# Performance work log

Hardware: AMD Instinct MI355X
Metric: run time of the kernel (lower is better)

## Reference

```python
import jax, jax.numpy as jnp
import numpy as np

EPS = 0.05
THRESH = 1e-6
MAX_ITER = 100


def _l2norm(x):
    # matches torch F.normalize(dim=-1): x / max(||x||, 1e-12)
    n = jnp.sqrt(jnp.sum(x * x, axis=-1, keepdims=True))
    return x / jnp.maximum(n, 1e-12)


def setup_inputs() -> dict:
    key = jax.random.key(0)
    kq, kk, kv = jax.random.split(key, 3)
    B, N, D = 8, 1024, 64
    return {
        "q": jax.random.normal(kq, (B, N, D), dtype=jnp.float32),
        "k": jax.random.normal(kk, (B, N, D), dtype=jnp.float32),
        "V": jax.random.normal(kv, (B, N, D), dtype=jnp.float32),
    }


def reference(q, k, V):
    B, N, D = q.shape
    Q = _l2norm(q)
    Kn = _l2norm(k)
    # cost matrix: 1 - cosine similarity, shape (B, N, N)
    C = 1.0 - jnp.einsum("bnd,bmd->bnm", Q, Kn)

    log_mu = jnp.full((B, N), jnp.log(1.0 / N + 1e-8), dtype=C.dtype)
    log_nu = log_mu

    def kernel(u, v):
        # (-C + u_i + v_j) / eps, shape (B, N, N)
        return (-C + u[:, :, None] + v[:, None, :]) / EPS

    def step(carry, _):
        u, v, done = carry
        u0 = u
        u_new = EPS * (log_mu - jax.scipy.special.logsumexp(kernel(u, v), axis=2)) + u
        v_new = EPS * (log_nu - jax.scipy.special.logsumexp(kernel(u_new, v), axis=1)) + v
        err = jnp.mean(jnp.abs(u_new - u0))
        # replicate torch early-break: once converged, freeze u, v
        u = jnp.where(done, u, u_new)
        v = jnp.where(done, v, v_new)
        done = jnp.logical_or(done, err < THRESH)
        return (u, v, done), None

    u0 = jnp.zeros((B, N), dtype=C.dtype)
    v0 = jnp.zeros((B, N), dtype=C.dtype)
    (u, v, _), _ = jax.lax.scan(
        jax.checkpoint(step), (u0, v0, jnp.array(False)), None, length=MAX_ITER
    )

    T = jnp.exp(kernel(u, v))  # transport plan (B, N, N)
    out = jnp.einsum("bnm,bmd->bnd", T, V) + V
    return out
```

## Files before the change

kernel.cpp:

```cpp
#include <hip/hip_runtime.h>
#include <math.h>

#define BB 8
#define NN 1024
#define DD 64
#define EPSF 0.05f
#define MAX_ITER 100
#define ERR_FX_THRESH 8590u
#define SCALE_ 28.853900817779268f
#define EPSLN2_ 0.034657359027997264f
#define NBLK 256
#define NPER 32

typedef __attribute__((ext_vector_type(8))) short short8;
typedef __attribute__((ext_vector_type(4))) float f32x4;

static __device__ __forceinline__ float fexp2(float x) { return __builtin_amdgcn_exp2f(x); }
static __device__ __forceinline__ float flog2(float x) { return __builtin_amdgcn_logf(x); }
static __device__ __forceinline__ float bflo(unsigned u) { return __uint_as_float(u << 16); }
static __device__ __forceinline__ unsigned short bf16rne(float x) {
    unsigned u = __float_as_uint(x);
    u += 0x7fffu + ((u >> 16) & 1u);
    return (unsigned short)(u >> 16);
}
__device__ __forceinline__ float wave_sum64(float x) {
#pragma unroll
    for (int off = 1; off < 64; off <<= 1) x += __shfl_xor(x, off);
    return x;
}

#define CNT64IDX(p, b) ((b) * 200 + (p))

__global__ __launch_bounds__(256) void cost_kernel(const float* __restrict__ q,
                                                   const float* __restrict__ k,
                                                   unsigned short* __restrict__ M,
                                                   unsigned short* __restrict__ MT) {
    __shared__ __align__(16) float Qs[64][65];
    __shared__ __align__(16) float Ks[64][65];
    __shared__ float qin[64];
    __shared__ float kin[64];
    __shared__ __align__(16) unsigned short Qb[64][72];
    __shared__ __align__(16) unsigned short Kb[64][72];
    int b = blockIdx.z;
    int i0 = blockIdx.y * 64, j0 = blockIdx.x * 64;
    const float* Qp = q + ((size_t)b * NN + i0) * DD;
    const float* Kp = k + ((size_t)b * NN + j0) * DD;
    int tid = threadIdx.x;
#pragma unroll
    for (int kk = 0; kk < 4; ++kk) {
        int c = tid + 256 * kk;
        int row = c >> 4;
        int c4 = c & 15;
        float4 qv = ((const float4*)(Qp + row * DD))[c4];
        Qs[row][c4 * 4 + 0] = qv.x; Qs[row][c4 * 4 + 1] = qv.y;
        Qs[row][c4 * 4 + 2] = qv.z; Qs[row][c4 * 4 + 3] = qv.w;
        float4 kv = ((const float4*)(Kp + row * DD))[c4];
        Ks[row][c4 * 4 + 0] = kv.x; Ks[row][c4 * 4 + 1] = kv.y;
        Ks[row][c4 * 4 + 2] = kv.z; Ks[row][c4 * 4 + 3] = kv.w;
    }
    __syncthreads();
    if (tid < 64) {
        float ss = 0.f;
#pragma unroll 16
        for (int d = 0; d < 64; ++d) ss += Qs[tid][d] * Qs[tid][d];
        qin[tid] = 1.0f / fmaxf(sqrtf(ss), 1e-12f);
    } else if (tid < 128) {
        int r = tid - 64;
        float ss = 0.f;
#pragma unroll 16
        for (int d = 0; d < 64; ++d) ss += Ks[r][d] * Ks[r][d];
        kin[r] = 1.0f / fmaxf(sqrtf(ss), 1e-12f);
    }
    __syncthreads();
    {
        int row = tid >> 2, d0 = (tid & 3) * 16;
        float qs = qin[row], ks = kin[row];
#pragma unroll
        for (int p = 0; p < 4; ++p) {
            int d = d0 + p * 4;
            uint2 t;
            t.x = (unsigned)bf16rne(Qs[row][d + 0] * qs) | ((unsigned)bf16rne(Qs[row][d + 1] * qs) << 16);
            t.y = (unsigned)bf16rne(Qs[row][d + 2] * qs) | ((unsigned)bf16rne(Qs[row][d + 3] * qs) << 16);
            *(uint2*)&Qb[row][d] = t;
            t.x = (unsigned)bf16rne(Ks[row][d + 0] * ks) | ((unsigned)bf16rne(Ks[row][d + 1] * ks) << 16);
            t.y = (unsigned)bf16rne(Ks[row][d + 2] * ks) | ((unsigned)bf16rne(Ks[row][d + 3] * ks) << 16);
            *(uint2*)&Kb[row][d] = t;
        }
    }
    __syncthreads();
    unsigned short* Ms = (unsigned short*)&Qs[0][0];
    int w = tid >> 6, lane = tid & 63;
    int m = lane & 15, qq = lane >> 4;
    int rloc = w * 16;
    short8 a0 = *(const short8*)&Qb[rloc + m][qq * 8];
    short8 a1 = *(const short8*)&Qb[rloc + m][qq * 8 + 32];
    f32x4 acc[4];
#pragma unroll
    for (int nt = 0; nt < 4; ++nt) {
        short8 b0 = *(const short8*)&Kb[nt * 16 + m][qq * 8];
        short8 b1 = *(const short8*)&Kb[nt * 16 + m][qq * 8 + 32];
        f32x4 z = {0.f, 0.f, 0.f, 0.f};
        z = __builtin_amdgcn_mfma_f32_16x16x32_bf16(a0, b0, z, 0, 0, 0);
        acc[nt] = __builtin_amdgcn_mfma_f32_16x16x32_bf16(a1, b1, z, 0, 0, 0);
    }
#pragma unroll
    for (int nt = 0; nt < 4; ++nt) {
        int gj = j0 + nt * 16 + m;
        unsigned short us[4];
#pragma unroll
        for (int r = 0; r < 4; ++r)
            us[r] = bf16rne(fexp2((acc[nt][r] - 1.0f) * SCALE_));
#pragma unroll
        for (int r = 0; r < 4; ++r)
            Ms[(rloc + qq * 4 + r) * 72 + nt * 16 + m] = us[r];
        uint2 t;
        t.x = (unsigned)us[0] | ((unsigned)us[1] << 16);
        t.y = (unsigned)us[2] | ((unsigned)us[3] << 16);
        *(uint2*)(MT + ((size_t)b << 20) + ((size_t)gj << 10) + i0 + rloc + qq * 4) = t;
    }
    __syncthreads();
#pragma unroll
    for (int s = 0; s < 2; ++s) {
        int idx = tid + 256 * s;
        int row = idx >> 3, seg = idx & 7;
        *(uint4*)(M + ((size_t)b << 20) + ((size_t)(i0 + row) << 10) + j0 + seg * 8) =
            *(const uint4*)&Ms[row * 72 + seg * 8];
    }
}

#define ACC8(U4, base)                                              \
    s0 = fmaf(bflo(U4.x), wrg[base + 0], s0);                       \
    s1 = fmaf(__uint_as_float(U4.x), wrg[base + 1], s1);            \
    s0 = fmaf(bflo(U4.y), wrg[base + 2], s0);                       \
    s1 = fmaf(__uint_as_float(U4.y), wrg[base + 3], s1);            \
    s0 = fmaf(bflo(U4.z), wrg[base + 4], s0);                       \
    s1 = fmaf(__uint_as_float(U4.z), wrg[base + 5], s1);            \
    s0 = fmaf(bflo(U4.w), wrg[base + 6], s0);                       \
    s1 = fmaf(__uint_as_float(U4.w), wrg[base + 7], s1);

__global__ __launch_bounds__(256, 1) void sink_coop(const unsigned short* __restrict__ M,
                                                    const unsigned short* __restrict__ MT,
                                                    float* __restrict__ u,
                                                    float* __restrict__ v,
                                                    unsigned long long* __restrict__ cnt64,
                                                    float eln) {
    __shared__ __align__(16) float sw[1280];
    __shared__ float sdel[4];
    __shared__ int sflag;
    int tid = threadIdx.x;
    int w = tid >> 6, lane = tid & 63;
    int b = blockIdx.x & 7;
    int slice = blockIdx.x >> 3;
    int rbase = slice * 32 + w * 8;
    const unsigned short* Mb  = M  + ((size_t)b << 20);
    const unsigned short* MTb = MT + ((size_t)b << 20);
    float* ub = u + (b << 10);
    float* vb = v + (b << 10);

    uint4 mA[8], mB[8], nA[8], nB[8];
#pragma unroll
    for (int r = 0; r < 8; ++r) {
        const uint4* rp = (const uint4*)(Mb + ((size_t)(rbase + r) << 10));
        mA[r] = rp[lane * 2];
        mB[r] = rp[lane * 2 + 1];
        const uint4* tp = (const uint4*)(MTb + ((size_t)(rbase + r) << 10));
        nA[r] = tp[lane * 2];
        nB[r] = tp[lane * 2 + 1];
    }

    float uprev[8];
#pragma unroll
    for (int r = 0; r < 8; ++r) uprev[r] = 0.f;

    unsigned myerr = 0xffffffffu;

    for (int t = 0; t < MAX_ITER; ++t) {
        {
            float4 ex;
            ex.x = fexp2(__hip_atomic_load(vb + tid * 4 + 0, __ATOMIC_RELAXED, __HIP_MEMORY_SCOPE_AGENT) * SCALE_);
            ex.y = fexp2(__hip_atomic_load(vb + tid * 4 + 1, __ATOMIC_RELAXED, __HIP_MEMORY_SCOPE_AGENT) * SCALE_);
            ex.z = fexp2(__hip_atomic_load(vb + tid * 4 + 2, __ATOMIC_RELAXED, __HIP_MEMORY_SCOPE_AGENT) * SCALE_);
            ex.w = fexp2(__hip_atomic_load(vb + tid * 4 + 3, __ATOMIC_RELAXED, __HIP_MEMORY_SCOPE_AGENT) * SCALE_);
            *(float4*)&sw[tid * 4 + 4 * (tid >> 2)] = ex;
            __syncthreads();
            float wrg[16];
            *(float4*)&wrg[0]  = *(const float4*)&sw[lane * 20 + 0];
            *(float4*)&wrg[4]  = *(const float4*)&sw[lane * 20 + 4];
            *(float4*)&wrg[8]  = *(const float4*)&sw[lane * 20 + 8];
            *(float4*)&wrg[12] = *(const float4*)&sw[lane * 20 + 12];
            float del = 0.f;
#pragma unroll
            for (int rr = 0; rr < 8; ++rr) {
                float s0 = 0.f, s1 = 0.f;
                ACC8(mA[rr], 0)
                ACC8(mB[rr], 8)
                float s = wave_sum64(s0 + s1);
                float un = eln - EPSLN2_ * flog2(s);
                del += fabsf(un - uprev[rr]);
                uprev[rr] = un;
                if (lane == 0)
                    __hip_atomic_store(ub + rbase + rr, un, __ATOMIC_RELAXED, __HIP_MEMORY_SCOPE_AGENT);
            }
            if (lane == 0) sdel[w] = del;
            asm volatile("s_waitcnt vmcnt(0)" ::: "memory");
            __syncthreads();
            if (tid == 0) {
                float dsum = sdel[0] + sdel[1] + sdel[2] + sdel[3];
                unsigned dfx = (unsigned)fminf(dsum * 1048576.0f, 6.0e7f) + 1u;
                unsigned long long* c = cnt64 + CNT64IDX(2 * t, b);
                unsigned long long tot =
                    __hip_atomic_fetch_add(c, (1ULL << 32) | (unsigned long long)dfx,
                                           __ATOMIC_RELAXED, __HIP_MEMORY_SCOPE_AGENT) +
                    ((1ULL << 32) | (unsigned long long)dfx);
                while ((unsigned)(tot >> 32) < NPER) {
                    __builtin_amdgcn_s_sleep(1);
                    tot = __hip_atomic_load(c, __ATOMIC_RELAXED, __HIP_MEMORY_SCOPE_AGENT);
                }
                myerr = (unsigned)tot;
            }
            __syncthreads();
        }
        {
            float4 ex;
            ex.x = fexp2(__hip_atomic_load(ub + tid * 4 + 0, __ATOMIC_RELAXED, __HIP_MEMORY_SCOPE_AGENT) * SCALE_);
            ex.y = fexp2(__hip_atomic_load(ub + tid * 4 + 1, __ATOMIC_RELAXED, __HIP_MEMORY_SCOPE_AGENT) * SCALE_);
            ex.z = fexp2(__hip_atomic_load(ub + tid * 4 + 2, __ATOMIC_RELAXED, __HIP_MEMORY_SCOPE_AGENT) * SCALE_);
            ex.w = fexp2(__hip_atomic_load(ub + tid * 4 + 3, __ATOMIC_RELAXED, __HIP_MEMORY_SCOPE_AGENT) * SCALE_);
            *(float4*)&sw[tid * 4 + 4 * (tid >> 2)] = ex;
            __syncthreads();
            float wrg[16];
            *(float4*)&wrg[0]  = *(const float4*)&sw[lane * 20 + 0];
            *(float4*)&wrg[4]  = *(const float4*)&sw[lane * 20 + 4];
            *(float4*)&wrg[8]  = *(const float4*)&sw[lane * 20 + 8];
            *(float4*)&wrg[12] = *(const float4*)&sw[lane * 20 + 12];
#pragma unroll
            for (int rr = 0; rr < 8; ++rr) {
                float s0 = 0.f, s1 = 0.f;
                ACC8(nA[rr], 0)
                ACC8(nB[rr], 8)
                float s = wave_sum64(s0 + s1);
                float vn = eln - EPSLN2_ * flog2(s);
                if (lane == 0)
                    __hip_atomic_store(vb + rbase + rr, vn, __ATOMIC_RELAXED, __HIP_MEMORY_SCOPE_AGENT);
            }
            asm volatile("s_waitcnt vmcnt(0)" ::: "memory");
            __syncthreads();
            if (tid == 0) {
                unsigned long long* c = cnt64 + CNT64IDX(2 * t + 1, b);
                unsigned long long tot =
                    __hip_atomic_fetch_add(c, 1ULL << 32, __ATOMIC_RELAXED, __HIP_MEMORY_SCOPE_AGENT) +
                    (1ULL << 32);
                while ((unsigned)(tot >> 32) < NPER) {
                    __builtin_amdgcn_s_sleep(1);
                    tot = __hip_atomic_load(c, __ATOMIC_RELAXED, __HIP_MEMORY_SCOPE_AGENT);
                }
                int brk = 0;
                if (myerr < ERR_FX_THRESH) {
                    unsigned long long s = 0;
                    for (int bb = 0; bb < 8; ++bb) {
                        unsigned long long tv = __hip_atomic_load(cnt64 + CNT64IDX(2 * t, bb),
                                                                  __ATOMIC_RELAXED, __HIP_MEMORY_SCOPE_AGENT);
                        while ((unsigned)(tv >> 32) < NPER) {
                            __builtin_amdgcn_s_sleep(1);
                            tv = __hip_atomic_load(cnt64 + CNT64IDX(2 * t, bb),
                                                   __ATOMIC_RELAXED, __HIP_MEMORY_SCOPE_AGENT);
                        }
                        s += (unsigned long long)(unsigned)tv;
                    }
                    brk = (s < (unsigned long long)ERR_FX_THRESH);
                }
                sflag = brk;
            }
            __syncthreads();
            if (sflag) break;
        }
    }
}

__global__ __launch_bounds__(256) void wt_kernel(const float* __restrict__ V,
                                                 const float* __restrict__ v,
                                                 unsigned short* __restrict__ WT) {
    __shared__ __align__(16) float Vs[64][65];
    __shared__ float wj[64];
    int b = blockIdx.x & 7, jt = blockIdx.x >> 3;
    int j0 = jt * 64;
    int tid = threadIdx.x;
    const float* Vb = V + ((size_t)b << 16) + ((size_t)j0 << 6);
#pragma unroll
    for (int c = 0; c < 4; ++c) {
        int idx = tid + 256 * c;
        int row = idx >> 4, c4 = idx & 15;
        float4 x = ((const float4*)(Vb + row * 64))[c4];
        Vs[row][c4 * 4 + 0] = x.x; Vs[row][c4 * 4 + 1] = x.y;
        Vs[row][c4 * 4 + 2] = x.z; Vs[row][c4 * 4 + 3] = x.w;
    }
    if (tid < 64) wj[tid] = fexp2(v[(b << 10) + j0 + tid] * SCALE_);
    __syncthreads();
    int d = tid >> 2, qd = tid & 3;
    unsigned pk[8];
#pragma unroll
    for (int p = 0; p < 8; ++p) {
        int j = qd * 16 + p * 2;
        unsigned lo = bf16rne(Vs[j][d] * wj[j]);
        unsigned hi = bf16rne(Vs[j + 1][d] * wj[j + 1]);
        pk[p] = lo | (hi << 16);
    }
    unsigned short* dst = WT + ((size_t)b << 16) + ((size_t)d << 10) + j0 + qd * 16;
    ((uint4*)dst)[0] = make_uint4(pk[0], pk[1], pk[2], pk[3]);
    ((uint4*)dst)[1] = make_uint4(pk[4], pk[5], pk[6], pk[7]);
}

__global__ __launch_bounds__(256) void gemm_final(const unsigned short* __restrict__ M,
                                                  const unsigned short* __restrict__ WT,
                                                  const float* __restrict__ u,
                                                  const float* __restrict__ V,
                                                  float* __restrict__ out) {
    __shared__ float sa[32];
    int tid = threadIdx.x;
    int w = tid >> 6, lane = tid & 63;
    int b = blockIdx.x & 7, mt = blockIdx.x >> 3;
    if (tid < 32) sa[tid] = fexp2(u[(b << 10) + mt * 32 + tid] * SCALE_);
    __syncthreads();
    int m = lane & 15, q = lane >> 4;
    int rloc = (w & 1) * 16;
    int nbase = (w >> 1) * 32;
    const unsigned short* Ma = M + ((size_t)b << 20) + ((size_t)(mt * 32 + rloc + m) << 10) + q * 8;
    const unsigned short* W0 = WT + ((size_t)b << 16) + ((size_t)(nbase + m) << 10) + q * 8;
    const unsigned short* W1 = W0 + (16 << 10);
    f32x4 acc0 = {0.f, 0.f, 0.f, 0.f}, acc1 = {0.f, 0.f, 0.f, 0.f};
#pragma unroll 4
    for (int k0 = 0; k0 < NN; k0 += 32) {
        short8 af = *(const short8*)(Ma + k0);
        short8 b0 = *(const short8*)(W0 + k0);
        short8 b1 = *(const short8*)(W1 + k0);
        acc0 = __builtin_amdgcn_mfma_f32_16x16x32_bf16(af, b0, acc0, 0, 0, 0);
        acc1 = __builtin_amdgcn_mfma_f32_16x16x32_bf16(af, b1, acc1, 0, 0, 0);
    }
#pragma unroll
    for (int r = 0; r < 4; ++r) {
        int lrow = rloc + q * 4 + r;
        int gm = mt * 32 + lrow;
        float a = sa[lrow];
        size_t base = (((size_t)b << 10) + gm) * DD;
        int n0 = nbase + m;
        out[base + n0]      = fmaf(a, acc0[r], V[base + n0]);
        out[base + n0 + 16] = fmaf(a, acc1[r], V[base + n0 + 16]);
    }
}

extern "C" void kernel_launch(void* const* d_in, const int* in_sizes, int n_in,
                              void* d_out, int out_size, void* d_ws, size_t ws_size,
                              hipStream_t stream) {
    const float* q = (const float*)d_in[0];
    const float* k = (const float*)d_in[1];
    const float* V = (const float*)d_in[2];
    float* out = (float*)d_out;

    char* ws = (char*)d_ws;
    const size_t MB16 = (size_t)BB * NN * NN * sizeof(unsigned short);
    unsigned short* M  = (unsigned short*)ws;
    unsigned short* MT = (unsigned short*)(ws + MB16);
    unsigned short* WT = MT;
    float* u   = (float*)(ws + 2 * MB16);
    float* v   = u + BB * NN;
    unsigned long long* cnt64 = (unsigned long long*)(v + BB * NN);

    size_t zbytes = (size_t)(2 * BB * NN) * 4 + 1600 * 8;
    hipMemsetAsync(u, 0, zbytes, stream);

    cost_kernel<<<dim3(16, 16, 8), 256, 0, stream>>>(q, k, M, MT);

    float eln = EPSF * logf(1.0f / NN + 1e-8f);
    sink_coop<<<dim3(NBLK), dim3(256), 0, stream>>>(M, MT, u, v, cnt64, eln);

    wt_kernel<<<128, 256, 0, stream>>>(V, v, WT);
    gemm_final<<<256, 256, 0, stream>>>(M, WT, u, V, out);
}
```

Baseline: 183.8 us.

## Replace barrier counters with epoch-tagged fixed-point u/v words for dataflow sync

The Sinkhorn cooperative kernel no longer uses per-half-iteration grid barriers. Each u/v entry is stored as a 32-bit word holding a 7-bit iteration tag and a 25-bit fixed-point value, so consumers spin on the data itself until all tags match. Wave 0 polls and decodes the values and hands them to the other waves through LDS flags. The convergence check is deferred by one iteration and overlapped with the next half-step. Together these remove barrier latency and block-wide syncthreads. The cost is quantized u/v values clamped to ±8, reliance on tag wraparound staying under 128 iterations, and busy-waiting in the LDS spin loops.

```diff
diff --git a/kernel.cpp b/kernel.cpp
--- a/kernel.cpp
+++ b/kernel.cpp
@@ -10,7 +10,9 @@
 #define SCALE_ 28.853900817779268f
 #define EPSLN2_ 0.034657359027997264f
 #define NBLK 256
-#define NPER 32
+#define NPERW 128
+#define QSCALE 2097152.0f
+#define DECE ((float)(28.853900817779268 / 2097152.0))
 
 typedef __attribute__((ext_vector_type(8))) short short8;
 typedef __attribute__((ext_vector_type(4))) float f32x4;
@@ -28,8 +30,11 @@
     for (int off = 1; off < 64; off <<= 1) x += __shfl_xor(x, off);
     return x;
 }
-
-#define CNT64IDX(p, b) ((b) * 200 + (p))
+static __device__ __forceinline__ float dec_exp(unsigned w) {
+    int fx = ((int)(w << 7)) >> 7;
+    return fexp2((float)fx * DECE);
+}
+
 
 __global__ __launch_bounds__(256) void cost_kernel(const float* __restrict__ q,
                                                    const float* __restrict__ k,
@@ -140,13 +145,13 @@
 
 __global__ __launch_bounds__(256, 1) void sink_coop(const unsigned short* __restrict__ M,
                                                     const unsigned short* __restrict__ MT,
-                                                    float* __restrict__ u,
-                                                    float* __restrict__ v,
+                                                    unsigned* __restrict__ ut,
+                                                    unsigned* __restrict__ vt,
                                                     unsigned long long* __restrict__ cnt64,
                                                     float eln) {
-    __shared__ __align__(16) float sw[1280];
-    __shared__ float sdel[4];
-    __shared__ int sflag;
+    __shared__ __align__(16) float bufU[1280];
+    __shared__ __align__(16) float bufV[1280];
+    __shared__ int flagU, flagV;
     int tid = threadIdx.x;
     int w = tid >> 6, lane = tid & 63;
     int b = blockIdx.x & 7;
@@ -154,8 +159,12 @@
     int rbase = slice * 32 + w * 8;
     const unsigned short* Mb  = M  + ((size_t)b << 20);
     const unsigned short* MTb = MT + ((size_t)b << 20);
-    float* ub = u + (b << 10);
-    float* vb = v + (b << 10);
+    unsigned* ub = ut + (b << 10);
+    unsigned* vb = vt + (b << 10);
+    const unsigned* vp = vb + lane * 16;
+    const unsigned* up = ub + lane * 16;
+
+    if (tid == 0) { flagU = 0; flagV = 0; }
 
     uint4 mA[8], mB[8], nA[8], nB[8];
 #pragma unroll
@@ -167,118 +176,149 @@
         nA[r] = tp[lane * 2];
         nB[r] = tp[lane * 2 + 1];
     }
+    __syncthreads();
 
     float uprev[8];
 #pragma unroll
     for (int r = 0; r < 8; ++r) uprev[r] = 0.f;
 
-    unsigned myerr = 0xffffffffu;
-
     for (int t = 0; t < MAX_ITER; ++t) {
-        {
-            float4 ex;
-            ex.x = fexp2(__hip_atomic_load(vb + tid * 4 + 0, __ATOMIC_RELAXED, __HIP_MEMORY_SCOPE_AGENT) * SCALE_);
-            ex.y = fexp2(__hip_atomic_load(vb + tid * 4 + 1, __ATOMIC_RELAXED, __HIP_MEMORY_SCOPE_AGENT) * SCALE_);
-            ex.z = fexp2(__hip_atomic_load(vb + tid * 4 + 2, __ATOMIC_RELAXED, __HIP_MEMORY_SCOPE_AGENT) * SCALE_);
-            ex.w = fexp2(__hip_atomic_load(vb + tid * 4 + 3, __ATOMIC_RELAXED, __HIP_MEMORY_SCOPE_AGENT) * SCALE_);
-            *(float4*)&sw[tid * 4 + 4 * (tid >> 2)] = ex;
-            __syncthreads();
-            float wrg[16];
-            *(float4*)&wrg[0]  = *(const float4*)&sw[lane * 20 + 0];
-            *(float4*)&wrg[4]  = *(const float4*)&sw[lane * 20 + 4];
-            *(float4*)&wrg[8]  = *(const float4*)&sw[lane * 20 + 8];
-            *(float4*)&wrg[12] = *(const float4*)&sw[lane * 20 + 12];
-            float del = 0.f;
-#pragma unroll
-            for (int rr = 0; rr < 8; ++rr) {
-                float s0 = 0.f, s1 = 0.f;
-                ACC8(mA[rr], 0)
-                ACC8(mB[rr], 8)
-                float s = wave_sum64(s0 + s1);
-                float un = eln - EPSLN2_ * flog2(s);
-                del += fabsf(un - uprev[rr]);
-                uprev[rr] = un;
-                if (lane == 0)
-                    __hip_atomic_store(ub + rbase + rr, un, __ATOMIC_RELAXED, __HIP_MEMORY_SCOPE_AGENT);
-            }
-            if (lane == 0) sdel[w] = del;
-            asm volatile("s_waitcnt vmcnt(0)" ::: "memory");
-            __syncthreads();
-            if (tid == 0) {
-                float dsum = sdel[0] + sdel[1] + sdel[2] + sdel[3];
-                unsigned dfx = (unsigned)fminf(dsum * 1048576.0f, 6.0e7f) + 1u;
-                unsigned long long* c = cnt64 + CNT64IDX(2 * t, b);
-                unsigned long long tot =
-                    __hip_atomic_fetch_add(c, (1ULL << 32) | (unsigned long long)dfx,
-                                           __ATOMIC_RELAXED, __HIP_MEMORY_SCOPE_AGENT) +
-                    ((1ULL << 32) | (unsigned long long)dfx);
-                while ((unsigned)(tot >> 32) < NPER) {
-                    __builtin_amdgcn_s_sleep(1);
-                    tot = __hip_atomic_load(c, __ATOMIC_RELAXED, __HIP_MEMORY_SCOPE_AGENT);
+        unsigned tgv = (unsigned)t;
+        unsigned tgu = (unsigned)(t + 1);
+        float wrg[16];
+        if (w == 0) {
+            unsigned wv[16];
+            for (;;) {
+                unsigned bad = 0;
+#pragma unroll
+                for (int i = 0; i < 16; ++i)
+                    wv[i] = __hip_atomic_load(vp + i, __ATOMIC_RELAXED, __HIP_MEMORY_SCOPE_AGENT);
+#pragma unroll
+                for (int i = 0; i < 16; ++i) bad |= (wv[i] >> 25) ^ tgv;
+                if (!bad) break;
+                __builtin_amdgcn_s_sleep(1);
+            }
+#pragma unroll
+            for (int i = 0; i < 4; ++i) {
+                float4 f;
+                f.x = dec_exp(wv[i * 4 + 0]); f.y = dec_exp(wv[i * 4 + 1]);
+                f.z = dec_exp(wv[i * 4 + 2]); f.w = dec_exp(wv[i * 4 + 3]);
+                *(float4*)&bufU[lane * 20 + i * 4] = f;
+                wrg[i * 4 + 0] = f.x; wrg[i * 4 + 1] = f.y;
+                wrg[i * 4 + 2] = f.z; wrg[i * 4 + 3] = f.w;
+            }
+            if (lane == 0)
+                __hip_atomic_store(&flagU, t + 1, __ATOMIC_RELEASE, __HIP_MEMORY_SCOPE_WORKGROUP);
+        } else {
+            while (__hip_atomic_load(&flagU, __ATOMIC_ACQUIRE, __HIP_MEMORY_SCOPE_WORKGROUP) < t + 1) {}
+#pragma unroll
+            for (int i = 0; i < 4; ++i) {
+                float4 f = *(const float4*)&bufU[lane * 20 + i * 4];
+                wrg[i * 4 + 0] = f.x; wrg[i * 4 + 1] = f.y;
+                wrg[i * 4 + 2] = f.z; wrg[i * 4 + 3] = f.w;
+            }
+        }
+        float del = 0.f;
+#pragma unroll
+        for (int rr = 0; rr < 8; ++rr) {
+            float s0 = 0.f, s1 = 0.f;
+            ACC8(mA[rr], 0)
+            ACC8(mB[rr], 8)
+            float s = wave_sum64(s0 + s1);
+            float un = eln - EPSLN2_ * flog2(s);
+            del += fabsf(un - uprev[rr]);
+            uprev[rr] = un;
+            if (lane == 0) {
+                float uq = fminf(fmaxf(un, -7.99f), 7.99f);
+                int fx = (int)rintf(uq * QSCALE);
+                unsigned word = (tgu << 25) | ((unsigned)fx & 0x1FFFFFFu);
+                __hip_atomic_store(ub + rbase + rr, word, __ATOMIC_RELAXED, __HIP_MEMORY_SCOPE_AGENT);
+            }
+        }
+        if (lane == 0) {
+            unsigned dfx = (unsigned)fminf(del * 1048576.0f, 1.5e7f) + 1u;
+            __hip_atomic_fetch_add(cnt64 + (size_t)t * 8 + b,
+                                   (1ULL << 32) | (unsigned long long)dfx,
+                                   __ATOMIC_RELAXED, __HIP_MEMORY_SCOPE_AGENT);
+        }
+        unsigned long long e[8];
+        if (t) {
+#pragma unroll
+            for (int i = 0; i < 8; ++i)
+                e[i] = __hip_atomic_load(cnt64 + (size_t)(t - 1) * 8 + i,
+                                         __ATOMIC_RELAXED, __HIP_MEMORY_SCOPE_AGENT);
+        }
+        if (w == 0) {
+            unsigned wu[16];
+            for (;;) {
+                unsigned bad = 0;
+#pragma unroll
+                for (int i = 0; i < 16; ++i)
+                    wu[i] = __hip_atomic_load(up + i, __ATOMIC_RELAXED, __HIP_MEMORY_SCOPE_AGENT);
+#pragma unroll
+                for (int i = 0; i < 16; ++i) bad |= (wu[i] >> 25) ^ tgu;
+                if (!bad) break;
+                __builtin_amdgcn_s_sleep(1);
+            }
+#pragma unroll
+            for (int i = 0; i < 4; ++i) {
+                float4 f;
+                f.x = dec_exp(wu[i * 4 + 0]); f.y = dec_exp(wu[i * 4 + 1]);
+                f.z = dec_exp(wu[i * 4 + 2]); f.w = dec_exp(wu[i * 4 + 3]);
+                *(float4*)&bufV[lane * 20 + i * 4] = f;
+                wrg[i * 4 + 0] = f.x; wrg[i * 4 + 1] = f.y;
+                wrg[i * 4 + 2] = f.z; wrg[i * 4 + 3] = f.w;
+            }
+            if (lane == 0)
+                __hip_atomic_store(&flagV, t + 1, __ATOMIC_RELEASE, __HIP_MEMORY_SCOPE_WORKGROUP);
+        } else {
+            while (__hip_atomic_load(&flagV, __ATOMIC_ACQUIRE, __HIP_MEMORY_SCOPE_WORKGROUP) < t + 1) {}
+#pragma unroll
+            for (int i = 0; i < 4; ++i) {
+                float4 f = *(const float4*)&bufV[lane * 20 + i * 4];
+                wrg[i * 4 + 0] = f.x; wrg[i * 4 + 1] = f.y;
+                wrg[i * 4 + 2] = f.z; wrg[i * 4 + 3] = f.w;
+            }
+        }
+#pragma unroll
+        for (int rr = 0; rr < 8; ++rr) {
+            float s0 = 0.f, s1 = 0.f;
+            ACC8(nA[rr], 0)
+            ACC8(nB[rr], 8)
+            float s = wave_sum64(s0 + s1);
+            float vn = eln - EPSLN2_ * flog2(s);
+            if (lane == 0) {
+                float vq = fminf(fmaxf(vn, -7.99f), 7.99f);
+                int fx = (int)rintf(vq * QSCALE);
+                unsigned word = (tgu << 25) | ((unsigned)fx & 0x1FFFFFFu);
+                __hip_atomic_store(vb + rbase + rr, word, __ATOMIC_RELAXED, __HIP_MEMORY_SCOPE_AGENT);
+            }
+        }
+        if (t) {
+            unsigned long long s = 0;
+            for (;;) {
+                unsigned mn = 0xffffffffu;
+                s = 0;
+#pragma unroll
+                for (int i = 0; i < 8; ++i) {
+                    unsigned c = (unsigned)(e[i] >> 32);
+                    if (c < mn) mn = c;
+                    s += (unsigned long long)(unsigned)(e[i] & 0xffffffffULL);
                 }
-                myerr = (unsigned)tot;
-            }
-            __syncthreads();
-        }
-        {
-            float4 ex;
-            ex.x = fexp2(__hip_atomic_load(ub + tid * 4 + 0, __ATOMIC_RELAXED, __HIP_MEMORY_SCOPE_AGENT) * SCALE_);
-            ex.y = fexp2(__hip_atomic_load(ub + tid * 4 + 1, __ATOMIC_RELAXED, __HIP_MEMORY_SCOPE_AGENT) * SCALE_);
-            ex.z = fexp2(__hip_atomic_load(ub + tid * 4 + 2, __ATOMIC_RELAXED, __HIP_MEMORY_SCOPE_AGENT) * SCALE_);
-            ex.w = fexp2(__hip_atomic_load(ub + tid * 4 + 3, __ATOMIC_RELAXED, __HIP_MEMORY_SCOPE_AGENT) * SCALE_);
-            *(float4*)&sw[tid * 4 + 4 * (tid >> 2)] = ex;
-            __syncthreads();
-            float wrg[16];
-            *(float4*)&wrg[0]  = *(const float4*)&sw[lane * 20 + 0];
-            *(float4*)&wrg[4]  = *(const float4*)&sw[lane * 20 + 4];
-            *(float4*)&wrg[8]  = *(const float4*)&sw[lane * 20 + 8];
-            *(float4*)&wrg[12] = *(const float4*)&sw[lane * 20 + 12];
-#pragma unroll
-            for (int rr = 0; rr < 8; ++rr) {
-                float s0 = 0.f, s1 = 0.f;
-                ACC8(nA[rr], 0)
-                ACC8(nB[rr], 8)
-                float s = wave_sum64(s0 + s1);
-                float vn = eln - EPSLN2_ * flog2(s);
-                if (lane == 0)
-                    __hip_atomic_store(vb + rbase + rr, vn, __ATOMIC_RELAXED, __HIP_MEMORY_SCOPE_AGENT);
-            }
-            asm volatile("s_waitcnt vmcnt(0)" ::: "memory");
-            __syncthreads();
-            if (tid == 0) {
-                unsigned long long* c = cnt64 + CNT64IDX(2 * t + 1, b);
-                unsigned long long tot =
-                    __hip_atomic_fetch_add(c, 1ULL << 32, __ATOMIC_RELAXED, __HIP_MEMORY_SCOPE_AGENT) +
-                    (1ULL << 32);
-                while ((unsigned)(tot >> 32) < NPER) {
-                    __builtin_amdgcn_s_sleep(1);
-                    tot = __hip_atomic_load(c, __ATOMIC_RELAXED, __HIP_MEMORY_SCOPE_AGENT);
-                }
-                int brk = 0;
-                if (myerr < ERR_FX_THRESH) {
-                    unsigned long long s = 0;
-                    for (int bb = 0; bb < 8; ++bb) {
-                        unsigned long long tv = __hip_atomic_load(cnt64 + CNT64IDX(2 * t, bb),
-                                                                  __ATOMIC_RELAXED, __HIP_MEMORY_SCOPE_AGENT);
-                        while ((unsigned)(tv >> 32) < NPER) {
-                            __builtin_amdgcn_s_sleep(1);
-                            tv = __hip_atomic_load(cnt64 + CNT64IDX(2 * t, bb),
-                                                   __ATOMIC_RELAXED, __HIP_MEMORY_SCOPE_AGENT);
-                        }
-                        s += (unsigned long long)(unsigned)tv;
-                    }
-                    brk = (s < (unsigned long long)ERR_FX_THRESH);
-                }
-                sflag = brk;
-            }
-            __syncthreads();
-            if (sflag) break;
+                if (mn >= NPERW) break;
+                __builtin_amdgcn_s_sleep(1);
+#pragma unroll
+                for (int i = 0; i < 8; ++i)
+                    e[i] = __hip_atomic_load(cnt64 + (size_t)(t - 1) * 8 + i,
+                                             __ATOMIC_RELAXED, __HIP_MEMORY_SCOPE_AGENT);
+            }
+            if (s < (unsigned long long)ERR_FX_THRESH) break;
         }
     }
 }
 
 __global__ __launch_bounds__(256) void wt_kernel(const float* __restrict__ V,
-                                                 const float* __restrict__ v,
+                                                 const unsigned* __restrict__ vt,
                                                  unsigned short* __restrict__ WT) {
     __shared__ __align__(16) float Vs[64][65];
     __shared__ float wj[64];
@@ -294,7 +334,7 @@
         Vs[row][c4 * 4 + 0] = x.x; Vs[row][c4 * 4 + 1] = x.y;
         Vs[row][c4 * 4 + 2] = x.z; Vs[row][c4 * 4 + 3] = x.w;
     }
-    if (tid < 64) wj[tid] = fexp2(v[(b << 10) + j0 + tid] * SCALE_);
+    if (tid < 64) wj[tid] = dec_exp(vt[(b << 10) + j0 + tid]);
     __syncthreads();
     int d = tid >> 2, qd = tid & 3;
     unsigned pk[8];
@@ -312,14 +352,14 @@
 
 __global__ __launch_bounds__(256) void gemm_final(const unsigned short* __restrict__ M,
                                                   const unsigned short* __restrict__ WT,
-                                                  const float* __restrict__ u,
+                                                  const unsigned* __restrict__ ut,
                                                   const float* __restrict__ V,
                                                   float* __restrict__ out) {
     __shared__ float sa[32];
     int tid = threadIdx.x;
     int w = tid >> 6, lane = tid & 63;
     int b = blockIdx.x & 7, mt = blockIdx.x >> 3;
-    if (tid < 32) sa[tid] = fexp2(u[(b << 10) + mt * 32 + tid] * SCALE_);
+    if (tid < 32) sa[tid] = dec_exp(ut[(b << 10) + mt * 32 + tid]);
     __syncthreads();
     int m = lane & 15, q = lane >> 4;
     int rloc = (w & 1) * 16;
@@ -361,18 +401,18 @@
     unsigned short* M  = (unsigned short*)ws;
     unsigned short* MT = (unsigned short*)(ws + MB16);
     unsigned short* WT = MT;
-    float* u   = (float*)(ws + 2 * MB16);
-    float* v   = u + BB * NN;
-    unsigned long long* cnt64 = (unsigned long long*)(v + BB * NN);
-
-    size_t zbytes = (size_t)(2 * BB * NN) * 4 + 1600 * 8;
-    hipMemsetAsync(u, 0, zbytes, stream);
+    unsigned* ut = (unsigned*)(ws + 2 * MB16);
+    unsigned* vt = ut + BB * NN;
+    unsigned long long* cnt64 = (unsigned long long*)(vt + BB * NN);
+
+    size_t zbytes = (size_t)(2 * BB * NN) * 4 + 800 * 8;
+    hipMemsetAsync(ut, 0, zbytes, stream);
 
     cost_kernel<<<dim3(16, 16, 8), 256, 0, stream>>>(q, k, M, MT);
 
     float eln = EPSF * logf(1.0f / NN + 1e-8f);
-    sink_coop<<<dim3(NBLK), dim3(256), 0, stream>>>(M, MT, u, v, cnt64, eln);
-
-    wt_kernel<<<128, 256, 0, stream>>>(V, v, WT);
-    gemm_final<<<256, 256, 0, stream>>>(M, WT, u, V, out);
-}
+    sink_coop<<<dim3(NBLK), dim3(256), 0, stream>>>(M, MT, ut, vt, cnt64, eln);
+
+    wt_kernel<<<128, 256, 0, stream>>>(V, vt, WT);
+    gemm_final<<<256, 256, 0, stream>>>(M, WT, ut, V, out);
+}
```

Measured after the change: 448.4 us. 144% more time.

## Replace per-block syncthreads barriers with LDS arrival counters and per-wave spinning

Applied to the files above, without the earlier changes.

Each wave now posts its error contribution and arrival into shared-memory atomic counters. The last-arriving wave issues the global grid-barrier atomic, and every wave spins on the global counter itself, so the two __syncthreads around the thread-0 barrier are gone. The exp-weight staging buffer is split into separate U and V buffers so consecutive phases do not overwrite each other without a block barrier. This is meant to cut intra-block barrier latency in the 200-phase cooperative loop, at the cost of four times as many waves polling global memory. The lack of acquire ordering between waves and the lower per-wave clamp on the error value may raise correctness or memory-ordering risks.

```diff
diff --git a/kernel.cpp b/kernel.cpp
--- a/kernel.cpp
+++ b/kernel.cpp
@@ -144,9 +144,10 @@
                                                     float* __restrict__ v,
                                                     unsigned long long* __restrict__ cnt64,
                                                     float eln) {
-    __shared__ __align__(16) float sw[1280];
-    __shared__ float sdel[4];
-    __shared__ int sflag;
+    __shared__ __align__(16) float bufU[1280];
+    __shared__ __align__(16) float bufV[1280];
+    __shared__ unsigned arr[2];
+    __shared__ unsigned ldsdel;
     int tid = threadIdx.x;
     int w = tid >> 6, lane = tid & 63;
     int b = blockIdx.x & 7;
@@ -157,6 +158,8 @@
     float* ub = u + (b << 10);
     float* vb = v + (b << 10);
 
+    if (tid == 0) { arr[0] = 0u; arr[1] = 0u; ldsdel = 0u; }
+
     uint4 mA[8], mB[8], nA[8], nB[8];
 #pragma unroll
     for (int r = 0; r < 8; ++r) {
@@ -167,6 +170,7 @@
         nA[r] = tp[lane * 2];
         nB[r] = tp[lane * 2 + 1];
     }
+    __syncthreads();
 
     float uprev[8];
 #pragma unroll
@@ -181,13 +185,13 @@
             ex.y = fexp2(__hip_atomic_load(vb + tid * 4 + 1, __ATOMIC_RELAXED, __HIP_MEMORY_SCOPE_AGENT) * SCALE_);
             ex.z = fexp2(__hip_atomic_load(vb + tid * 4 + 2, __ATOMIC_RELAXED, __HIP_MEMORY_SCOPE_AGENT) * SCALE_);
             ex.w = fexp2(__hip_atomic_load(vb + tid * 4 + 3, __ATOMIC_RELAXED, __HIP_MEMORY_SCOPE_AGENT) * SCALE_);
-            *(float4*)&sw[tid * 4 + 4 * (tid >> 2)] = ex;
+            *(float4*)&bufU[tid * 4 + 4 * (tid >> 2)] = ex;
             __syncthreads();
             float wrg[16];
-            *(float4*)&wrg[0]  = *(const float4*)&sw[lane * 20 + 0];
-            *(float4*)&wrg[4]  = *(const float4*)&sw[lane * 20 + 4];
-            *(float4*)&wrg[8]  = *(const float4*)&sw[lane * 20 + 8];
-            *(float4*)&wrg[12] = *(const float4*)&sw[lane * 20 + 12];
+            *(float4*)&wrg[0]  = *(const float4*)&bufU[lane * 20 + 0];
+            *(float4*)&wrg[4]  = *(const float4*)&bufU[lane * 20 + 4];
+            *(float4*)&wrg[8]  = *(const float4*)&bufU[lane * 20 + 8];
+            *(float4*)&wrg[12] = *(const float4*)&bufU[lane * 20 + 12];
             float del = 0.f;
 #pragma unroll
             for (int rr = 0; rr < 8; ++rr) {
@@ -201,24 +205,26 @@
                 if (lane == 0)
                     __hip_atomic_store(ub + rbase + rr, un, __ATOMIC_RELAXED, __HIP_MEMORY_SCOPE_AGENT);
             }
-            if (lane == 0) sdel[w] = del;
             asm volatile("s_waitcnt vmcnt(0)" ::: "memory");
-            __syncthreads();
-            if (tid == 0) {
-                float dsum = sdel[0] + sdel[1] + sdel[2] + sdel[3];
-                unsigned dfx = (unsigned)fminf(dsum * 1048576.0f, 6.0e7f) + 1u;
-                unsigned long long* c = cnt64 + CNT64IDX(2 * t, b);
-                unsigned long long tot =
-                    __hip_atomic_fetch_add(c, (1ULL << 32) | (unsigned long long)dfx,
-                                           __ATOMIC_RELAXED, __HIP_MEMORY_SCOPE_AGENT) +
-                    ((1ULL << 32) | (unsigned long long)dfx);
-                while ((unsigned)(tot >> 32) < NPER) {
-                    __builtin_amdgcn_s_sleep(1);
-                    tot = __hip_atomic_load(c, __ATOMIC_RELAXED, __HIP_MEMORY_SCOPE_AGENT);
+            unsigned long long* c = cnt64 + CNT64IDX(2 * t, b);
+            if (lane == 0) {
+                unsigned dfx = (unsigned)fminf(del * 1048576.0f, 1.5e7f) + 1u;
+                __hip_atomic_fetch_add(&ldsdel, dfx, __ATOMIC_RELAXED, __HIP_MEMORY_SCOPE_WORKGROUP);
+                unsigned old = __hip_atomic_fetch_add(&arr[0], 1u, __ATOMIC_ACQ_REL, __HIP_MEMORY_SCOPE_WORKGROUP);
+                if (old == 3u) {
+                    unsigned ds = __hip_atomic_load(&ldsdel, __ATOMIC_RELAXED, __HIP_MEMORY_SCOPE_WORKGROUP);
+                    __hip_atomic_store(&ldsdel, 0u, __ATOMIC_RELAXED, __HIP_MEMORY_SCOPE_WORKGROUP);
+                    __hip_atomic_store(&arr[0], 0u, __ATOMIC_RELAXED, __HIP_MEMORY_SCOPE_WORKGROUP);
+                    __hip_atomic_fetch_add(c, (1ULL << 32) | (unsigned long long)ds,
+                                           __ATOMIC_RELAXED, __HIP_MEMORY_SCOPE_AGENT);
                 }
-                myerr = (unsigned)tot;
-            }
-            __syncthreads();
+            }
+            unsigned long long tot = __hip_atomic_load(c, __ATOMIC_RELAXED, __HIP_MEMORY_SCOPE_AGENT);
+            while ((unsigned)(tot >> 32) < NPER) {
+                __builtin_amdgcn_s_sleep(1);
+                tot = __hip_atomic_load(c, __ATOMIC_RELAXED, __HIP_MEMORY_SCOPE_AGENT);
+            }
+            myerr = (unsigned)tot;
         }
         {
             float4 ex;
@@ -226,13 +232,13 @@
             ex.y = fexp2(__hip_atomic_load(ub + tid * 4 + 1, __ATOMIC_RELAXED, __HIP_MEMORY_SCOPE_AGENT) * SCALE_);
             ex.z = fexp2(__hip_atomic_load(ub + tid * 4 + 2, __ATOMIC_RELAXED, __HIP_MEMORY_SCOPE_AGENT) * SCALE_);
             ex.w = fexp2(__hip_atomic_load(ub + tid * 4 + 3, __ATOMIC_RELAXED, __HIP_MEMORY_SCOPE_AGENT) * SCALE_);
-            *(float4*)&sw[tid * 4 + 4 * (tid >> 2)] = ex;
+            *(float4*)&bufV[tid * 4 + 4 * (tid >> 2)] = ex;
             __syncthreads();
             float wrg[16];
-            *(float4*)&wrg[0]  = *(const float4*)&sw[lane * 20 + 0];
-            *(float4*)&wrg[4]  = *(const float4*)&sw[lane * 20 + 4];
-            *(float4*)&wrg[8]  = *(const float4*)&sw[lane * 20 + 8];
-            *(float4*)&wrg[12] = *(const float4*)&sw[lane * 20 + 12];
+            *(float4*)&wrg[0]  = *(const float4*)&bufV[lane * 20 + 0];
+            *(float4*)&wrg[4]  = *(const float4*)&bufV[lane * 20 + 4];
+            *(float4*)&wrg[8]  = *(const float4*)&bufV[lane * 20 + 8];
+            *(float4*)&wrg[12] = *(const float4*)&bufV[lane * 20 + 12];
 #pragma unroll
             for (int rr = 0; rr < 8; ++rr) {
                 float s0 = 0.f, s1 = 0.f;
@@ -244,35 +250,34 @@
                     __hip_atomic_store(vb + rbase + rr, vn, __ATOMIC_RELAXED, __HIP_MEMORY_SCOPE_AGENT);
             }
             asm volatile("s_waitcnt vmcnt(0)" ::: "memory");
-            __syncthreads();
-            if (tid == 0) {
-                unsigned long long* c = cnt64 + CNT64IDX(2 * t + 1, b);
-                unsigned long long tot =
-                    __hip_atomic_fetch_add(c, 1ULL << 32, __ATOMIC_RELAXED, __HIP_MEMORY_SCOPE_AGENT) +
-                    (1ULL << 32);
-                while ((unsigned)(tot >> 32) < NPER) {
-                    __builtin_amdgcn_s_sleep(1);
-                    tot = __hip_atomic_load(c, __ATOMIC_RELAXED, __HIP_MEMORY_SCOPE_AGENT);
+            unsigned long long* c = cnt64 + CNT64IDX(2 * t + 1, b);
+            if (lane == 0) {
+                unsigned old = __hip_atomic_fetch_add(&arr[1], 1u, __ATOMIC_ACQ_REL, __HIP_MEMORY_SCOPE_WORKGROUP);
+                if (old == 3u) {
+                    __hip_atomic_store(&arr[1], 0u, __ATOMIC_RELAXED, __HIP_MEMORY_SCOPE_WORKGROUP);
+                    __hip_atomic_fetch_add(c, 1ULL << 32,
+                                           __ATOMIC_RELAXED, __HIP_MEMORY_SCOPE_AGENT);
                 }
-                int brk = 0;
-                if (myerr < ERR_FX_THRESH) {
-                    unsigned long long s = 0;
-                    for (int bb = 0; bb < 8; ++bb) {
-                        unsigned long long tv = __hip_atomic_load(cnt64 + CNT64IDX(2 * t, bb),
-                                                                  __ATOMIC_RELAXED, __HIP_MEMORY_SCOPE_AGENT);
-                        while ((unsigned)(tv >> 32) < NPER) {
-                            __builtin_amdgcn_s_sleep(1);
-                            tv = __hip_atomic_load(cnt64 + CNT64IDX(2 * t, bb),
-                                                   __ATOMIC_RELAXED, __HIP_MEMORY_SCOPE_AGENT);
-                        }
-                        s += (unsigned long long)(unsigned)tv;
+            }
+            unsigned long long tot = __hip_atomic_load(c, __ATOMIC_RELAXED, __HIP_MEMORY_SCOPE_AGENT);
+            while ((unsigned)(tot >> 32) < NPER) {
+                __builtin_amdgcn_s_sleep(1);
+                tot = __hip_atomic_load(c, __ATOMIC_RELAXED, __HIP_MEMORY_SCOPE_AGENT);
+            }
+            if (myerr < ERR_FX_THRESH) {
+                unsigned long long s = 0;
+                for (int bb = 0; bb < 8; ++bb) {
+                    unsigned long long tv = __hip_atomic_load(cnt64 + CNT64IDX(2 * t, bb),
+                                                              __ATOMIC_RELAXED, __HIP_MEMORY_SCOPE_AGENT);
+                    while ((unsigned)(tv >> 32) < NPER) {
+                        __builtin_amdgcn_s_sleep(1);
+                        tv = __hip_atomic_load(cnt64 + CNT64IDX(2 * t, bb),
+                                               __ATOMIC_RELAXED, __HIP_MEMORY_SCOPE_AGENT);
                     }
-                    brk = (s < (unsigned long long)ERR_FX_THRESH);
+                    s += (unsigned long long)(unsigned)tv;
                 }
-                sflag = brk;
-            }
-            __syncthreads();
-            if (sflag) break;
+                if (s < (unsigned long long)ERR_FX_THRESH) break;
+            }
         }
     }
 }
```

Measured after the change: 233.8 us. +27.2%, slower.
